# Kernel tuning notes

Hardware: AMD Instinct MI355X
Metric: run time of the kernel (lower is better)

The kernel has to match this reference:

```python
import jax, jax.numpy as jnp
import numpy as np

B, C = 16, 256          # batch, feature_dim
P, K = 20, 50           # max_polygons, max_points
H4 = W4 = 32            # p4 spatial
H2 = W2 = 128           # p2 spatial


def setup_inputs() -> dict:
    key = jax.random.key(0)
    ks = jax.random.split(key, 12)

    def w(k, shape, fan_in):
        return jax.random.normal(k, shape, jnp.float32) * (1.0 / np.sqrt(fan_in))

    return {
        "p4": jax.random.normal(ks[0], (B, C, H4, W4), jnp.float32),
        "p2": jax.random.normal(ks[1], (B, C, H2, W2), jnp.float32),
        "segmentation": jax.random.uniform(ks[2], (B, 1, H2, W2), dtype=jnp.float32),
        # init_net linears (torch layout: [out, in])
        "W1": w(ks[3], (1024, C * 64), C * 64), "b1": jnp.zeros((1024,), jnp.float32),
        "W2": w(ks[4], (P * K * 2, 1024), 1024), "b2": jnp.zeros((P * K * 2,), jnp.float32),
        # refine_net
        "R1": w(ks[5], (128, C + 2), C + 2), "rb1": jnp.zeros((128,), jnp.float32),
        "R2": w(ks[6], (64, 128), 128), "rb2": jnp.zeros((64,), jnp.float32),
        "R3": w(ks[7], (2, 64), 64), "rb3": jnp.zeros((2,), jnp.float32),
        # validity_net
        "V1": w(ks[8], (128, K * 2), K * 2), "vb1": jnp.zeros((128,), jnp.float32),
        "V2": w(ks[9], (1, 128), 128), "vb2": jnp.zeros((1,), jnp.float32),
    }


def _bilinear_sample(img, xy):
    """F.grid_sample(align_corners=False, padding='zeros') for one image.
    img: [C, H, W]; xy: [N, 2] in [-1, 1] with xy[:, 0]=x (width), xy[:, 1]=y (height).
    Returns [N, C]."""
    Cc, H, W = img.shape
    x = ((xy[:, 0] + 1.0) * W - 1.0) * 0.5
    y = ((xy[:, 1] + 1.0) * H - 1.0) * 0.5
    x0 = jnp.floor(x)
    y0 = jnp.floor(y)
    wx1 = x - x0
    wy1 = y - y0

    def corner(xi, yi, wgt):
        valid = (xi >= 0) & (xi <= W - 1) & (yi >= 0) & (yi <= H - 1)
        xc = jnp.clip(xi, 0, W - 1).astype(jnp.int32)
        yc = jnp.clip(yi, 0, H - 1).astype(jnp.int32)
        v = img[:, yc, xc]  # [C, N]
        return v * (wgt * valid.astype(img.dtype))[None, :]

    out = (corner(x0, y0, (1 - wx1) * (1 - wy1))
           + corner(x0 + 1, y0, wx1 * (1 - wy1))
           + corner(x0, y0 + 1, (1 - wx1) * wy1)
           + corner(x0 + 1, y0 + 1, wx1 * wy1))
    return out.T  # [N, C]


def reference(p4, p2, segmentation, W1, b1, W2, b2, R1, rb1, R2, rb2, R3, rb3, V1, vb1, V2, vb2):
    Bn, Cc, h4, w4 = p4.shape
    pooled = p4.reshape(Bn, Cc, 8, h4 // 8, 8, w4 // 8).mean(axis=(3, 5))
    flat = pooled.reshape(Bn, -1)                       # [B, C*64]
    h = jax.nn.relu(flat @ W1.T + b1)
    init_pts = jax.nn.sigmoid(h @ W2.T + b2).reshape(Bn, P, K, 2)

    # refine: grid_sample point gather + 3-layer MLP
    grid = init_pts * 2.0 - 1.0                          # [B, P, K, 2]
    xy = grid.reshape(Bn, -1, 2)                         # [B, N=P*K, 2]
    sampled = jax.vmap(_bilinear_sample)(p2, xy)         # [B, N, C]
    coords = init_pts.reshape(Bn, -1, 2)
    feat = jnp.concatenate([sampled, coords], axis=-1)   # [B, N, C+2]
    h1 = jax.nn.relu(feat @ R1.T + rb1)
    h2 = jax.nn.relu(h1 @ R2.T + rb2)
    disp = jnp.tanh(h2 @ R3.T + rb3).reshape(Bn, P, K, 2)
    refined = jnp.clip(init_pts + 0.1 * disp, 0.0, 1.0)

    # validity
    pf = refined.reshape(Bn * P, K * 2)
    v = jax.nn.sigmoid(jax.nn.relu(pf @ V1.T + vb1) @ V2.T + vb2).reshape(Bn, P)
    return refined, v, init_pts
```

## Files before the change

### kernel.cpp

```cpp
#include <hip/hip_runtime.h>
#include <hip/hip_bf16.h>
#include <math.h>

#define NB 16
#define NC 256
#define NPTS 1000
#define NN2 2000
#define D1 1024
#define KFLAT 16384

__global__ __launch_bounds__(256) void k_prep(const float* __restrict__ R1,
                                              const float* __restrict__ R2,
                                              const float* __restrict__ V1,
                                              float* __restrict__ R1t,
                                              float* __restrict__ R2t_g,
                                              float* __restrict__ V1t_g) {
    int idx = blockIdx.x * 256 + threadIdx.x;
    if (idx < 33024) {
        int j = idx / 258, k = idx % 258;
        R1t[k * 128 + j] = R1[idx];
    } else if (idx < 33024 + 8192) {
        int t = idx - 33024;
        int j = t >> 7, k = t & 127;
        R2t_g[k * 64 + j] = R2[t];
    } else if (idx < 33024 + 8192 + 12800) {
        int t = idx - 41216;
        int j = t / 100, k = t % 100;
        V1t_g[k * 128 + j] = V1[t];
    }
}

__global__ __launch_bounds__(256) void k_pool(const float* __restrict__ p4,
                                              float* __restrict__ flat) {
    int o = blockIdx.x * 256 + threadIdx.x;
    int bc = o >> 6;
    int ij = o & 63;
    int i = ij >> 3, j = ij & 7;
    const float* src = p4 + ((size_t)bc * 32 + i * 4) * 32 + j * 4;
    float s = 0.f;
#pragma unroll
    for (int di = 0; di < 4; ++di) {
        float4 v = *reinterpret_cast<const float4*>(src + di * 32);
        s += v.x + v.y + v.z + v.w;
    }
    flat[o] = s * (1.0f / 16.0f);
}

__global__ __launch_bounds__(512) void k_fc1(const float* __restrict__ flat,
                                             const float* __restrict__ W1,
                                             const float* __restrict__ b1,
                                             float* __restrict__ h) {
    __shared__ float lds[2 * 16 * 256];
    const int tid = threadIdx.x;
    const int wave = tid >> 6, lane = tid & 63;
    const int colw = wave & 3, half = wave >> 2;
    const int n = blockIdx.x * 4 + colw;
    float acc[16];
#pragma unroll
    for (int m = 0; m < 16; ++m) acc[m] = 0.f;
    const float4* W1r  = reinterpret_cast<const float4*>(W1 + (size_t)n * KFLAT + half * 8192);
    const float4* flat4 = reinterpret_cast<const float4*>(flat);
    float4* lds4 = reinterpret_cast<float4*>(lds);
    for (int kt = 0; kt < 8192; kt += 256) {
        __syncthreads();
#pragma unroll
        for (int r = 0; r < 4; ++r) {
            int idx4 = tid + r * 512;
            int hh = idx4 >> 10;
            int m  = (idx4 >> 6) & 15;
            int off = idx4 & 63;
            lds4[idx4] = flat4[m * 4096 + hh * 2048 + (kt >> 2) + off];
        }
        __syncthreads();
        float4 w = W1r[(kt >> 2) + lane];
#pragma unroll
        for (int m = 0; m < 16; ++m) {
            float4 f = lds4[half * 1024 + m * 64 + lane];
            acc[m] += w.x * f.x + w.y * f.y + w.z * f.z + w.w * f.w;
        }
    }
#pragma unroll
    for (int m = 0; m < 16; ++m) {
        float v = acc[m];
#pragma unroll
        for (int off = 32; off > 0; off >>= 1) v += __shfl_xor(v, off, 64);
        acc[m] = v;
    }
    __syncthreads();
    if (lane == 0) {
#pragma unroll
        for (int m = 0; m < 16; ++m) lds[wave * 16 + m] = acc[m];
    }
    __syncthreads();
    if (tid < 64) {
        int c = tid >> 4, m = tid & 15;
        float v = lds[c * 16 + m] + lds[(c + 4) * 16 + m] + b1[blockIdx.x * 4 + c];
        h[m * D1 + blockIdx.x * 4 + c] = fmaxf(v, 0.f);
    }
}

__global__ __launch_bounds__(256) void k_fc2(const float* __restrict__ h,
                                             const float* __restrict__ W2,
                                             const float* __restrict__ b2,
                                             float* __restrict__ init_ws,
                                             float* __restrict__ out_init) {
    const int tid = threadIdx.x;
    const int wave = tid >> 6, lane = tid & 63;
    const int n = blockIdx.x * 4 + wave;
    float acc[16];
#pragma unroll
    for (int m = 0; m < 16; ++m) acc[m] = 0.f;
    const float4* W2r = reinterpret_cast<const float4*>(W2 + (size_t)n * D1);
    const float4* h4  = reinterpret_cast<const float4*>(h);
#pragma unroll
    for (int it = 0; it < 4; ++it) {
        int k4 = it * 64 + lane;
        float4 w = W2r[k4];
#pragma unroll
        for (int m = 0; m < 16; ++m) {
            float4 f = h4[m * 256 + k4];
            acc[m] += w.x * f.x + w.y * f.y + w.z * f.z + w.w * f.w;
        }
    }
    float bias = b2[n];
#pragma unroll
    for (int m = 0; m < 16; ++m) {
        float v = acc[m];
#pragma unroll
        for (int off = 32; off > 0; off >>= 1) v += __shfl_xor(v, off, 64);
        if (lane == 0) {
            float s = 1.f / (1.f + expf(-(v + bias)));
            init_ws[m * NN2 + n] = s;
            out_init[m * NN2 + n] = s;
        }
    }
}

__global__ __launch_bounds__(256) void k_sample(const float* __restrict__ p2,
                                                const float* __restrict__ init_ws,
                                                __hip_bfloat16* __restrict__ sampled) {
    __shared__ float img[128 * 128];
    const int bc = blockIdx.x;
    const int b = bc >> 8;
    const float4* src4 = reinterpret_cast<const float4*>(p2 + (size_t)bc * 16384);
    float4* dst4 = reinterpret_cast<float4*>(img);
#pragma unroll
    for (int i = 0; i < 16; ++i)
        dst4[threadIdx.x + i * 256] = src4[threadIdx.x + i * 256];
    __syncthreads();
    const float* ip = init_ws + b * NN2;
    for (int n = threadIdx.x; n < NPTS; n += 256) {
        float sx = ip[2 * n], sy = ip[2 * n + 1];
        float x = sx * 128.f - 0.5f;
        float y = sy * 128.f - 0.5f;
        float x0f = floorf(x), y0f = floorf(y);
        float wx = x - x0f, wy = y - y0f;
        int x0 = (int)x0f, y0 = (int)y0f;
        int x1 = x0 + 1, y1 = y0 + 1;
        bool vx0 = (x0 >= 0) && (x0 <= 127);
        bool vx1 = (x1 >= 0) && (x1 <= 127);
        bool vy0 = (y0 >= 0) && (y0 <= 127);
        bool vy1 = (y1 >= 0) && (y1 <= 127);
        int cx0 = min(max(x0, 0), 127), cx1 = min(max(x1, 0), 127);
        int cy0 = min(max(y0, 0), 127), cy1 = min(max(y1, 0), 127);
        float v00 = (vx0 && vy0) ? img[cy0 * 128 + cx0] : 0.f;
        float v10 = (vx1 && vy0) ? img[cy0 * 128 + cx1] : 0.f;
        float v01 = (vx0 && vy1) ? img[cy1 * 128 + cx0] : 0.f;
        float v11 = (vx1 && vy1) ? img[cy1 * 128 + cx1] : 0.f;
        float r = v00 * (1.f - wx) * (1.f - wy) + v10 * wx * (1.f - wy)
                + v01 * (1.f - wx) * wy + v11 * wx * wy;
        sampled[(size_t)bc * NPTS + n] = __float2bfloat16(r);
    }
}

__global__ __launch_bounds__(256) void k_r1(const __hip_bfloat16* __restrict__ sampled,
                                            const float* __restrict__ init_ws,
                                            const float* __restrict__ R1t,
                                            const float* __restrict__ rb1,
                                            float* __restrict__ h1) {
    __shared__ float As[64][128];
    __shared__ float Bs[64][32];
    const int tid = threadIdx.x;
    const int b = blockIdx.x >> 5;
    const int n0 = (blockIdx.x & 31) * 32;
    const int jt = tid & 15;
    const int nt = tid >> 4;
    float acc[8][2];
#pragma unroll
    for (int a = 0; a < 8; ++a) { acc[a][0] = 0.f; acc[a][1] = 0.f; }

    for (int k0 = 0; k0 < 256; k0 += 64) {
        __syncthreads();
        for (int idx = tid; idx < 128 * 64; idx += 256) {
            int kk = idx >> 7, r = idx & 127;
            As[kk][r] = R1t[(k0 + kk) * 128 + r];
        }
        for (int idx = tid; idx < 64 * 32; idx += 256) {
            int r = idx >> 5, col = idx & 31;
            int n = n0 + col;
            Bs[r][col] = (n < NPTS)
                ? __bfloat162float(sampled[((size_t)(b * 256 + k0 + r)) * NPTS + n])
                : 0.f;
        }
        __syncthreads();
#pragma unroll 8
        for (int kk = 0; kk < 64; ++kk) {
            float4 a0 = *reinterpret_cast<const float4*>(&As[kk][jt * 4]);
            float4 a1 = *reinterpret_cast<const float4*>(&As[kk][64 + jt * 4]);
            float2 bb = *reinterpret_cast<const float2*>(&Bs[kk][nt * 2]);
            float av[8] = {a0.x, a0.y, a0.z, a0.w, a1.x, a1.y, a1.z, a1.w};
            float bv[2] = {bb.x, bb.y};
#pragma unroll
            for (int a = 0; a < 8; ++a) {
                acc[a][0] += av[a] * bv[0];
                acc[a][1] += av[a] * bv[1];
            }
        }
    }
    float xs[2] = {0, 0}, ys[2] = {0, 0};
    int ns[2];
#pragma unroll
    for (int m = 0; m < 2; ++m) {
        int n = n0 + nt * 2 + m;
        ns[m] = n;
        if (n < NPTS) {
            xs[m] = init_ws[b * NN2 + 2 * n];
            ys[m] = init_ws[b * NN2 + 2 * n + 1];
        }
    }
#pragma unroll
    for (int a = 0; a < 8; ++a) {
        int j = (a < 4) ? (jt * 4 + a) : (64 + jt * 4 + (a - 4));
        float rx = R1t[256 * 128 + j];
        float ry = R1t[257 * 128 + j];
        float bj = rb1[j];
#pragma unroll
        for (int m = 0; m < 2; ++m) {
            int n = ns[m];
            if (n < NPTS) {
                float v = acc[a][m] + rx * xs[m] + ry * ys[m] + bj;
                h1[((size_t)(b * NPTS + n)) * 128 + j] = fmaxf(v, 0.f);
            }
        }
    }
}

__global__ __launch_bounds__(256) void k_r23(const float* __restrict__ h1,
                                             const float* __restrict__ init_ws,
                                             const float* __restrict__ R2t_g,
                                             const float* __restrict__ rb2,
                                             const float* __restrict__ R3,
                                             const float* __restrict__ rb3,
                                             float* __restrict__ refined) {
    const int tid = threadIdx.x, wave = tid >> 6, lane = tid & 63;
    const int wgid = blockIdx.x * 4 + wave;
    const int n = wgid & 1023;
    const int bbase = (wgid >> 10) * 8;
    if (n >= 1000) return;

    __shared__ float R2t[128][64];
    __shared__ float r3[2][64];
    __shared__ float rb2s[64];
    __shared__ float hbuf[4][128];
    for (int idx = tid; idx < 128 * 64; idx += 256)
        R2t[idx >> 6][idx & 63] = R2t_g[idx];
    if (tid < 128) r3[tid >> 6][tid & 63] = R3[tid];
    if (tid < 64) rb2s[tid] = rb2[tid];

    float hA[8], hB[8];
#pragma unroll
    for (int it = 0; it < 8; ++it) {
        size_t pt = (size_t)(bbase + it) * 1000 + n;
        hA[it] = h1[pt * 128 + lane];
        hB[it] = h1[pt * 128 + 64 + lane];
    }
    __syncthreads();
    const float b30 = rb3[0], b31 = rb3[1];
#pragma unroll
    for (int it = 0; it < 8; ++it) {
        int bb = bbase + it;
        size_t pt = (size_t)bb * 1000 + n;
        __syncthreads();
        hbuf[wave][lane] = hA[it];
        hbuf[wave][64 + lane] = hB[it];
        __syncthreads();
        float a = rb2s[lane];
#pragma unroll 16
        for (int k = 0; k < 128; ++k)
            a += R2t[k][lane] * hbuf[wave][k];
        a = fmaxf(a, 0.f);
        float d0 = r3[0][lane] * a;
        float d1 = r3[1][lane] * a;
#pragma unroll
        for (int off = 32; off > 0; off >>= 1) {
            d0 += __shfl_xor(d0, off, 64);
            d1 += __shfl_xor(d1, off, 64);
        }
        if (lane == 0) {
            float ix = init_ws[bb * NN2 + 2 * n];
            float iy = init_ws[bb * NN2 + 2 * n + 1];
            float rx = ix + 0.1f * tanhf(d0 + b30);
            float ry = iy + 0.1f * tanhf(d1 + b31);
            refined[pt * 2]     = fminf(fmaxf(rx, 0.f), 1.f);
            refined[pt * 2 + 1] = fminf(fmaxf(ry, 0.f), 1.f);
        }
    }
}

__global__ __launch_bounds__(256) void k_vhead(const float* __restrict__ refined,
                                               const float* __restrict__ V1t_g,
                                               const float* __restrict__ vb1,
                                               const float* __restrict__ V2,
                                               const float* __restrict__ vb2,
                                               float* __restrict__ vout) {
    __shared__ float V1t[100][128];
    __shared__ float pf[4][100];
    const int tid = threadIdx.x, wave = tid >> 6, lane = tid & 63;
    for (int idx = tid; idx < 100 * 128; idx += 256)
        V1t[idx >> 7][idx & 127] = V1t_g[idx];
    __syncthreads();
    const int row = blockIdx.x * 4 + wave;
    const float* src = refined + row * 100;
    if (lane < 50) {
        pf[wave][lane] = src[lane];
        pf[wave][lane + 50] = src[lane + 50];
    }
    __syncthreads();
    float a0 = vb1[lane], a1 = vb1[64 + lane];
#pragma unroll 10
    for (int k = 0; k < 100; ++k) {
        float p = pf[wave][k];
        a0 += V1t[k][lane] * p;
        a1 += V1t[k][64 + lane] * p;
    }
    float s = fmaxf(a0, 0.f) * V2[lane] + fmaxf(a1, 0.f) * V2[64 + lane];
#pragma unroll
    for (int off = 32; off > 0; off >>= 1) s += __shfl_xor(s, off, 64);
    if (lane == 0) vout[row] = 1.f / (1.f + expf(-(s + vb2[0])));
}

extern "C" void kernel_launch(void* const* d_in, const int* in_sizes, int n_in,
                              void* d_out, int out_size, void* d_ws, size_t ws_size,
                              hipStream_t stream) {
    const float* p4  = (const float*)d_in[0];
    const float* p2  = (const float*)d_in[1];
    const float* W1  = (const float*)d_in[3];
    const float* b1  = (const float*)d_in[4];
    const float* W2  = (const float*)d_in[5];
    const float* b2  = (const float*)d_in[6];
    const float* R1  = (const float*)d_in[7];
    const float* rb1 = (const float*)d_in[8];
    const float* R2  = (const float*)d_in[9];
    const float* rb2 = (const float*)d_in[10];
    const float* R3  = (const float*)d_in[11];
    const float* rb3 = (const float*)d_in[12];
    const float* V1  = (const float*)d_in[13];
    const float* vb1 = (const float*)d_in[14];
    const float* V2  = (const float*)d_in[15];
    const float* vb2 = (const float*)d_in[16];
    float* out = (float*)d_out;

    char* ws = (char*)d_ws;
    float* flat = (float*)(ws + 0);
    float* h    = (float*)(ws + 1048576);
    float* ipts = (float*)(ws + 1114112);
    float* h1   = (float*)(ws + 1242112);
    __hip_bfloat16* samp = (__hip_bfloat16*)(ws + 9434112);
    float* R1t  = (float*)(ws + 17626112);
    float* R2t_g= (float*)(ws + 17758208);
    float* V1t_g= (float*)(ws + 17790976);

    k_prep<<<212, 256, 0, stream>>>(R1, R2, V1, R1t, R2t_g, V1t_g);
    k_pool<<<1024, 256, 0, stream>>>(p4, flat);
    k_fc1<<<256, 512, 0, stream>>>(flat, W1, b1, h);
    k_fc2<<<500, 256, 0, stream>>>(h, W2, b2, ipts, out + 32320);
    k_sample<<<4096, 256, 0, stream>>>(p2, ipts, samp);
    k_r1<<<512, 256, 0, stream>>>(samp, ipts, R1t, rb1, h1);
    k_r23<<<512, 256, 0, stream>>>(h1, ipts, R2t_g, rb2, R3, rb3, out);
    k_vhead<<<80, 256, 0, stream>>>(out, V1t_g, vb1, V2, vb2, out + 32000);
}
```

Measured before the change: 584.3 us.

## Store pooled features as bf16, restructure sampling, and transpose refine MLP layout

Pooled p4 features are written as bf16 and fc1 reads them via 8-wide vector loads with register prefetch of the next W1 chunk, halving activation traffic. k_sample uses 1024-thread blocks so each thread handles one point. k_r1 now writes h1 transposed (feature-major), and k_r23 is rewritten as one thread per point holding 128 hidden values in registers and doing the 128x64 layer from global R2t, replacing the LDS/shuffle scheme. The bf16 activations lose precision, and the per-thread register-heavy k_r23 risks spills and low occupancy with only 256 single-wave blocks.

Measured after the change: 641.1 us. 9.7% more time.

```diff
diff --git a/kernel.cpp b/kernel.cpp
--- a/kernel.cpp
+++ b/kernel.cpp
@@ -8,6 +8,14 @@
 #define NN2 2000
 #define D1 1024
 #define KFLAT 16384
+
+typedef unsigned short ushort8 __attribute__((ext_vector_type(8)));
+
+static __device__ __forceinline__ float bf2f(unsigned short v) {
+    union { unsigned int u; float f; } x;
+    x.u = ((unsigned int)v) << 16;
+    return x.f;
+}
 
 __global__ __launch_bounds__(256) void k_prep(const float* __restrict__ R1,
                                               const float* __restrict__ R2,
@@ -31,7 +39,7 @@
 }
 
 __global__ __launch_bounds__(256) void k_pool(const float* __restrict__ p4,
-                                              float* __restrict__ flat) {
+                                              __hip_bfloat16* __restrict__ flat_bf) {
     int o = blockIdx.x * 256 + threadIdx.x;
     int bc = o >> 6;
     int ij = o & 63;
@@ -43,14 +51,15 @@
         float4 v = *reinterpret_cast<const float4*>(src + di * 32);
         s += v.x + v.y + v.z + v.w;
     }
-    flat[o] = s * (1.0f / 16.0f);
-}
-
-__global__ __launch_bounds__(512) void k_fc1(const float* __restrict__ flat,
+    flat_bf[o] = __float2bfloat16(s * (1.0f / 16.0f));
+}
+
+__global__ __launch_bounds__(512) void k_fc1(const __hip_bfloat16* __restrict__ flat_bf,
                                              const float* __restrict__ W1,
                                              const float* __restrict__ b1,
                                              float* __restrict__ h) {
-    __shared__ float lds[2 * 16 * 256];
+    __shared__ unsigned short tile[2 * 16 * 512];
+    __shared__ float red[8 * 16];
     const int tid = threadIdx.x;
     const int wave = tid >> 6, lane = tid & 63;
     const int colw = wave & 3, half = wave >> 2;
@@ -58,26 +67,35 @@
     float acc[16];
 #pragma unroll
     for (int m = 0; m < 16; ++m) acc[m] = 0.f;
-    const float4* W1r  = reinterpret_cast<const float4*>(W1 + (size_t)n * KFLAT + half * 8192);
-    const float4* flat4 = reinterpret_cast<const float4*>(flat);
-    float4* lds4 = reinterpret_cast<float4*>(lds);
-    for (int kt = 0; kt < 8192; kt += 256) {
+    const float4* W1r4 = reinterpret_cast<const float4*>(W1 + (size_t)n * KFLAT + half * 8192);
+    const ushort8* flat8 = reinterpret_cast<const ushort8*>(flat_bf);
+    ushort8* tile8 = reinterpret_cast<ushort8*>(tile);
+
+    float4 wa = W1r4[lane * 2], wb = W1r4[lane * 2 + 1];
+    for (int it = 0; it < 16; ++it) {
         __syncthreads();
 #pragma unroll
         for (int r = 0; r < 4; ++r) {
-            int idx4 = tid + r * 512;
-            int hh = idx4 >> 10;
-            int m  = (idx4 >> 6) & 15;
-            int off = idx4 & 63;
-            lds4[idx4] = flat4[m * 4096 + hh * 2048 + (kt >> 2) + off];
+            int idx = tid + r * 512;
+            int hh = idx >> 10, m = (idx >> 6) & 15, off = idx & 63;
+            tile8[idx] = flat8[m * 2048 + hh * 1024 + it * 64 + off];
         }
         __syncthreads();
-        float4 w = W1r[(kt >> 2) + lane];
+        float4 na = wa, nb = wb;
+        if (it < 15) {
+            na = W1r4[(it + 1) * 128 + lane * 2];
+            nb = W1r4[(it + 1) * 128 + lane * 2 + 1];
+        }
 #pragma unroll
         for (int m = 0; m < 16; ++m) {
-            float4 f = lds4[half * 1024 + m * 64 + lane];
-            acc[m] += w.x * f.x + w.y * f.y + w.z * f.z + w.w * f.w;
-        }
+            ushort8 u = tile8[half * 1024 + m * 64 + lane];
+            float s = wa.x * bf2f(u.s0) + wa.y * bf2f(u.s1)
+                    + wa.z * bf2f(u.s2) + wa.w * bf2f(u.s3)
+                    + wb.x * bf2f(u.s4) + wb.y * bf2f(u.s5)
+                    + wb.z * bf2f(u.s6) + wb.w * bf2f(u.s7);
+            acc[m] += s;
+        }
+        wa = na; wb = nb;
     }
 #pragma unroll
     for (int m = 0; m < 16; ++m) {
@@ -89,12 +107,12 @@
     __syncthreads();
     if (lane == 0) {
 #pragma unroll
-        for (int m = 0; m < 16; ++m) lds[wave * 16 + m] = acc[m];
+        for (int m = 0; m < 16; ++m) red[wave * 16 + m] = acc[m];
     }
     __syncthreads();
     if (tid < 64) {
         int c = tid >> 4, m = tid & 15;
-        float v = lds[c * 16 + m] + lds[(c + 4) * 16 + m] + b1[blockIdx.x * 4 + c];
+        float v = red[c * 16 + m] + red[(c + 4) * 16 + m] + b1[blockIdx.x * 4 + c];
         h[m * D1 + blockIdx.x * 4 + c] = fmaxf(v, 0.f);
     }
 }
@@ -136,23 +154,24 @@
     }
 }
 
-__global__ __launch_bounds__(256) void k_sample(const float* __restrict__ p2,
-                                                const float* __restrict__ init_ws,
-                                                __hip_bfloat16* __restrict__ sampled) {
+__global__ __launch_bounds__(1024) void k_sample(const float* __restrict__ p2,
+                                                 const float* __restrict__ init_ws,
+                                                 __hip_bfloat16* __restrict__ sampled) {
     __shared__ float img[128 * 128];
     const int bc = blockIdx.x;
     const int b = bc >> 8;
     const float4* src4 = reinterpret_cast<const float4*>(p2 + (size_t)bc * 16384);
     float4* dst4 = reinterpret_cast<float4*>(img);
 #pragma unroll
-    for (int i = 0; i < 16; ++i)
-        dst4[threadIdx.x + i * 256] = src4[threadIdx.x + i * 256];
+    for (int i = 0; i < 4; ++i)
+        dst4[threadIdx.x + i * 1024] = src4[threadIdx.x + i * 1024];
     __syncthreads();
     const float* ip = init_ws + b * NN2;
-    for (int n = threadIdx.x; n < NPTS; n += 256) {
-        float sx = ip[2 * n], sy = ip[2 * n + 1];
-        float x = sx * 128.f - 0.5f;
-        float y = sy * 128.f - 0.5f;
+    const int n = threadIdx.x;
+    if (n < NPTS) {
+        float2 sxy = *reinterpret_cast<const float2*>(ip + 2 * n);
+        float x = sxy.x * 128.f - 0.5f;
+        float y = sxy.y * 128.f - 0.5f;
         float x0f = floorf(x), y0f = floorf(y);
         float wx = x - x0f, wy = y - y0f;
         int x0 = (int)x0f, y0 = (int)y0f;
@@ -177,14 +196,14 @@
                                             const float* __restrict__ init_ws,
                                             const float* __restrict__ R1t,
                                             const float* __restrict__ rb1,
-                                            float* __restrict__ h1) {
+                                            float* __restrict__ h1t) {
     __shared__ float As[64][128];
     __shared__ float Bs[64][32];
     const int tid = threadIdx.x;
     const int b = blockIdx.x >> 5;
     const int n0 = (blockIdx.x & 31) * 32;
-    const int jt = tid & 15;
-    const int nt = tid >> 4;
+    const int nt = tid & 15;
+    const int jt = tid >> 4;
     float acc[8][2];
 #pragma unroll
     for (int a = 0; a < 8; ++a) { acc[a][0] = 0.f; acc[a][1] = 0.f; }
@@ -209,101 +228,78 @@
             float4 a1 = *reinterpret_cast<const float4*>(&As[kk][64 + jt * 4]);
             float2 bb = *reinterpret_cast<const float2*>(&Bs[kk][nt * 2]);
             float av[8] = {a0.x, a0.y, a0.z, a0.w, a1.x, a1.y, a1.z, a1.w};
-            float bv[2] = {bb.x, bb.y};
 #pragma unroll
             for (int a = 0; a < 8; ++a) {
-                acc[a][0] += av[a] * bv[0];
-                acc[a][1] += av[a] * bv[1];
+                acc[a][0] += av[a] * bb.x;
+                acc[a][1] += av[a] * bb.y;
             }
         }
     }
-    float xs[2] = {0, 0}, ys[2] = {0, 0};
-    int ns[2];
-#pragma unroll
-    for (int m = 0; m < 2; ++m) {
-        int n = n0 + nt * 2 + m;
-        ns[m] = n;
-        if (n < NPTS) {
-            xs[m] = init_ws[b * NN2 + 2 * n];
-            ys[m] = init_ws[b * NN2 + 2 * n + 1];
-        }
-    }
+    const int npair = n0 + nt * 2;
+    float4 c4 = make_float4(0.f, 0.f, 0.f, 0.f);
+    if (npair < NPTS)
+        c4 = *reinterpret_cast<const float4*>(init_ws + b * NN2 + 2 * npair);
 #pragma unroll
     for (int a = 0; a < 8; ++a) {
         int j = (a < 4) ? (jt * 4 + a) : (64 + jt * 4 + (a - 4));
         float rx = R1t[256 * 128 + j];
         float ry = R1t[257 * 128 + j];
         float bj = rb1[j];
-#pragma unroll
-        for (int m = 0; m < 2; ++m) {
-            int n = ns[m];
-            if (n < NPTS) {
-                float v = acc[a][m] + rx * xs[m] + ry * ys[m] + bj;
-                h1[((size_t)(b * NPTS + n)) * 128 + j] = fmaxf(v, 0.f);
-            }
-        }
-    }
-}
-
-__global__ __launch_bounds__(256) void k_r23(const float* __restrict__ h1,
-                                             const float* __restrict__ init_ws,
-                                             const float* __restrict__ R2t_g,
-                                             const float* __restrict__ rb2,
-                                             const float* __restrict__ R3,
-                                             const float* __restrict__ rb3,
-                                             float* __restrict__ refined) {
-    const int tid = threadIdx.x, wave = tid >> 6, lane = tid & 63;
-    const int wgid = blockIdx.x * 4 + wave;
-    const int n = wgid & 1023;
-    const int bbase = (wgid >> 10) * 8;
-    if (n >= 1000) return;
-
-    __shared__ float R2t[128][64];
-    __shared__ float r3[2][64];
-    __shared__ float rb2s[64];
-    __shared__ float hbuf[4][128];
-    for (int idx = tid; idx < 128 * 64; idx += 256)
-        R2t[idx >> 6][idx & 63] = R2t_g[idx];
-    if (tid < 128) r3[tid >> 6][tid & 63] = R3[tid];
-    if (tid < 64) rb2s[tid] = rb2[tid];
-
-    float hA[8], hB[8];
-#pragma unroll
-    for (int it = 0; it < 8; ++it) {
-        size_t pt = (size_t)(bbase + it) * 1000 + n;
-        hA[it] = h1[pt * 128 + lane];
-        hB[it] = h1[pt * 128 + 64 + lane];
-    }
-    __syncthreads();
-    const float b30 = rb3[0], b31 = rb3[1];
-#pragma unroll
-    for (int it = 0; it < 8; ++it) {
-        int bb = bbase + it;
-        size_t pt = (size_t)bb * 1000 + n;
-        __syncthreads();
-        hbuf[wave][lane] = hA[it];
-        hbuf[wave][64 + lane] = hB[it];
-        __syncthreads();
-        float a = rb2s[lane];
-#pragma unroll 16
-        for (int k = 0; k < 128; ++k)
-            a += R2t[k][lane] * hbuf[wave][k];
-        a = fmaxf(a, 0.f);
-        float d0 = r3[0][lane] * a;
-        float d1 = r3[1][lane] * a;
-#pragma unroll
-        for (int off = 32; off > 0; off >>= 1) {
-            d0 += __shfl_xor(d0, off, 64);
-            d1 += __shfl_xor(d1, off, 64);
-        }
-        if (lane == 0) {
-            float ix = init_ws[bb * NN2 + 2 * n];
-            float iy = init_ws[bb * NN2 + 2 * n + 1];
-            float rx = ix + 0.1f * tanhf(d0 + b30);
-            float ry = iy + 0.1f * tanhf(d1 + b31);
-            refined[pt * 2]     = fminf(fmaxf(rx, 0.f), 1.f);
-            refined[pt * 2 + 1] = fminf(fmaxf(ry, 0.f), 1.f);
-        }
+        float v0 = fmaxf(acc[a][0] + rx * c4.x + ry * c4.y + bj, 0.f);
+        float v1 = fmaxf(acc[a][1] + rx * c4.z + ry * c4.w + bj, 0.f);
+        if (npair < NPTS) {
+            float2 st = make_float2(v0, v1);
+            *reinterpret_cast<float2*>(h1t + ((size_t)(b * 128 + j)) * NPTS + npair) = st;
+        }
+    }
+}
+
+__global__ __launch_bounds__(64) void k_r23(const float* __restrict__ h1t,
+                                            const float* __restrict__ init_ws,
+                                            const float* __restrict__ R2t_g,
+                                            const float* __restrict__ rb2,
+                                            const float* __restrict__ R3,
+                                            const float* __restrict__ rb3,
+                                            float* __restrict__ refined) {
+    const int lane = threadIdx.x;
+    const int wid = blockIdx.x;
+    const int b = wid >> 4;
+    const int n = (wid & 15) * 64 + lane;
+    const bool act = (n < NPTS);
+    const int nc = act ? n : (NPTS - 1);
+
+    float hreg[128];
+    const float* hp = h1t + (size_t)b * (128 * NPTS) + nc;
+#pragma unroll
+    for (int k = 0; k < 128; ++k) hreg[k] = hp[(size_t)k * NPTS];
+
+    float acc[64];
+#pragma unroll
+    for (int j = 0; j < 64; ++j) acc[j] = rb2[j];
+
+#pragma unroll
+    for (int k = 0; k < 128; ++k) {
+        const float* wr = R2t_g + k * 64;
+#pragma unroll
+        for (int j = 0; j < 64; ++j)
+            acc[j] = fmaf(wr[j], hreg[k], acc[j]);
+    }
+
+    float d0 = 0.f, d1 = 0.f;
+#pragma unroll
+    for (int j = 0; j < 64; ++j) {
+        float a = fmaxf(acc[j], 0.f);
+        d0 = fmaf(R3[j], a, d0);
+        d1 = fmaf(R3[64 + j], a, d1);
+    }
+    float2 ip = *reinterpret_cast<const float2*>(init_ws + b * NN2 + 2 * nc);
+    float rx = ip.x + 0.1f * tanhf(d0 + rb3[0]);
+    float ry = ip.y + 0.1f * tanhf(d1 + rb3[1]);
+    rx = fminf(fmaxf(rx, 0.f), 1.f);
+    ry = fminf(fmaxf(ry, 0.f), 1.f);
+    if (act) {
+        float2 st = make_float2(rx, ry);
+        *reinterpret_cast<float2*>(refined + ((size_t)b * NPTS + n) * 2) = st;
     }
 }
 
@@ -361,21 +357,21 @@
     float* out = (float*)d_out;
 
     char* ws = (char*)d_ws;
-    float* flat = (float*)(ws + 0);
-    float* h    = (float*)(ws + 1048576);
-    float* ipts = (float*)(ws + 1114112);
-    float* h1   = (float*)(ws + 1242112);
-    __hip_bfloat16* samp = (__hip_bfloat16*)(ws + 9434112);
-    float* R1t  = (float*)(ws + 17626112);
-    float* R2t_g= (float*)(ws + 17758208);
-    float* V1t_g= (float*)(ws + 17790976);
+    __hip_bfloat16* flat_bf = (__hip_bfloat16*)(ws + 0);
+    float* h    = (float*)(ws + 524288);
+    float* ipts = (float*)(ws + 589824);
+    float* h1t  = (float*)(ws + 717824);
+    __hip_bfloat16* samp = (__hip_bfloat16*)(ws + 8909824);
+    float* R1t  = (float*)(ws + 17101824);
+    float* R2t_g= (float*)(ws + 17233920);
+    float* V1t_g= (float*)(ws + 17266688);
 
     k_prep<<<212, 256, 0, stream>>>(R1, R2, V1, R1t, R2t_g, V1t_g);
-    k_pool<<<1024, 256, 0, stream>>>(p4, flat);
-    k_fc1<<<256, 512, 0, stream>>>(flat, W1, b1, h);
+    k_pool<<<1024, 256, 0, stream>>>(p4, flat_bf);
+    k_fc1<<<256, 512, 0, stream>>>(flat_bf, W1, b1, h);
     k_fc2<<<500, 256, 0, stream>>>(h, W2, b2, ipts, out + 32320);
-    k_sample<<<4096, 256, 0, stream>>>(p2, ipts, samp);
-    k_r1<<<512, 256, 0, stream>>>(samp, ipts, R1t, rb1, h1);
-    k_r23<<<512, 256, 0, stream>>>(h1, ipts, R2t_g, rb2, R3, rb3, out);
+    k_sample<<<4096, 1024, 0, stream>>>(p2, ipts, samp);
+    k_r1<<<512, 256, 0, stream>>>(samp, ipts, R1t, rb1, h1t);
+    k_r23<<<256, 64, 0, stream>>>(h1t, ipts, R2t_g, rb2, R3, rb3, out);
     k_vhead<<<80, 256, 0, stream>>>(out, V1t_g, vb1, V2, vb2, out + 32000);
 }
```
